# Performance work log

Measured on AMD Instinct MI355X. Metric: run time of the kernel, lower is better.

## Reference

```python
import jax, jax.numpy as jnp
import numpy as np

EPS = 1e-3  # BatchNorm eps from module init
N, C_IN, K = 200000, 256, 27
C_MID = C_IN // 4  # bottleneck expansion = 4


def batch_norm(h, gamma, beta):
    # BatchNorm1d in training mode: biased batch stats over the node dim
    mean = jnp.mean(h, axis=0)
    var = jnp.var(h, axis=0)
    return (h - mean) * jax.lax.rsqrt(var + EPS) * gamma + beta


def setup_inputs() -> dict:
    key = jax.random.key(0)
    ks = jax.random.split(key, 8)
    x = jax.random.normal(ks[0], (N, C_IN), dtype=jnp.float32)
    neigh = jax.random.randint(ks[1], (N, K), 0, N)  # 27-neighbor octree table
    # conv weights (no bias; BN follows). Fan-in scaled init.
    W1 = jax.random.normal(ks[2], (C_IN, C_MID), dtype=jnp.float32) / np.sqrt(C_IN)
    W2 = jax.random.normal(ks[3], (K, C_MID, C_MID), dtype=jnp.float32) / np.sqrt(K * C_MID)
    W3 = jax.random.normal(ks[4], (C_MID, C_IN), dtype=jnp.float32) / np.sqrt(C_MID)
    g1 = jnp.ones((C_MID,), jnp.float32); b1 = jnp.zeros((C_MID,), jnp.float32)
    g2 = jnp.ones((C_MID,), jnp.float32); b2 = jnp.zeros((C_MID,), jnp.float32)
    g3 = jnp.ones((C_IN,), jnp.float32); b3 = jnp.zeros((C_IN,), jnp.float32)
    return {"x": x, "neigh": neigh, "depth": 6,
            "W1": W1, "g1": g1, "b1": b1,
            "W2": W2, "g2": g2, "b2": b2,
            "W3": W3, "g3": g3, "b3": b3}


def reference(x, neigh, depth, W1, g1, b1, W2, g2, b2, W3, g3, b3):
    identity = x
    # conv_bn_relu1: 1x1 octree conv -> BN -> ReLU
    h = jax.nn.relu(batch_norm(x @ W1, g1, b1))  # [N, C_MID]
    # conv_bn_relu2: 3x3 octree conv (27-neighbor gather) -> BN -> ReLU
    gathered = h[neigh]                          # [N, 27, C_MID] irregular gather
    h = jnp.einsum('nkc,kcd->nd', gathered, W2)  # [N, C_MID]
    h = jax.nn.relu(batch_norm(h, g2, b2))
    # conv3: 1x1 octree conv back to C_IN, then BN + residual + ReLU
    h = batch_norm(h @ W3, g3, b3)               # [N, C_IN]
    return jax.nn.relu(h + identity)
```

## Files before the change

kernel.cpp:

```cpp
#include <hip/hip_runtime.h>
#include <stdint.h>

#define N_NODES 200000
#define C_INN   256
#define C_MIDD  64
#define KNB     27
#define MB_TILES 3125
#define GRAM_BLOCKS 512

typedef unsigned short u16;
typedef __attribute__((ext_vector_type(8))) short short8;
typedef __attribute__((ext_vector_type(4))) float floatx4;

__device__ inline float bf2f(u16 u) {
  union { uint32_t i; float f; } v; v.i = ((uint32_t)u) << 16; return v.f;
}
__device__ inline u16 f2bf(float f) {
  union { float f; uint32_t i; } v; v.f = f;
  uint32_t lsb = (v.i >> 16) & 1u;
  uint32_t r = v.i + 0x7fffu + lsb;
  return (u16)(r >> 16);
}

__global__ void prep_kernel(const float* __restrict__ W1, const float* __restrict__ W2,
                            const float* __restrict__ W3,
                            u16* __restrict__ w1t, u16* __restrict__ w2t,
                            u16* __restrict__ w3t, float* __restrict__ stats) {
  int tid = blockIdx.x * blockDim.x + threadIdx.x;
  int nth = gridDim.x * blockDim.x;
  for (int i = tid; i < 512; i += nth) stats[i] = 0.f;
  for (int i = tid; i < 256 * 64; i += nth) {
    int d = i >> 8, k = i & 255;
    w1t[i] = f2bf(W1[k * 64 + d]);
  }
  for (int i = tid; i < 27 * 64 * 64; i += nth) {
    int kn = i >> 12, r = i & 4095, d = r >> 6, c = r & 63;
    w2t[i] = f2bf(W2[kn * 4096 + c * 64 + d]);
  }
  for (int i = tid; i < 256 * 64; i += nth) {
    int d = i >> 6, k = i & 63;
    w3t[i] = f2bf(W3[k * 256 + d]);
  }
}

#define PAD1 136
__global__ __launch_bounds__(256) void gemm1_kernel(const float* __restrict__ x,
                                                    const u16* __restrict__ w1t,
                                                    u16* __restrict__ y1,
                                                    float* __restrict__ s) {
  __shared__ u16 Als[64 * PAD1];
  __shared__ u16 Bls[64 * PAD1];
  int t = threadIdx.x;
  long long rowBase = (long long)blockIdx.x * 64;
  int w = t >> 6, lane = t & 63;
  int m = lane & 15, q = lane >> 4;
  floatx4 acc[4] = {};

  for (int kh = 0; kh < 2; kh++) {
    if (kh) __syncthreads();
    #pragma unroll
    for (int j = 0; j < 8; j++) {
      int lin = j * 256 + t;
      int r = lin >> 5, c4 = lin & 31;
      floatx4 v = ((const floatx4*)x)[(rowBase + r) * 64 + kh * 32 + c4];
      ushort4 u;
      u.x = f2bf(v[0]); u.y = f2bf(v[1]); u.z = f2bf(v[2]); u.w = f2bf(v[3]);
      *(ushort4*)&Als[r * PAD1 + c4 * 4] = u;
    }
    #pragma unroll
    for (int j = 0; j < 4; j++) {
      int lin = j * 256 + t;
      int n = lin >> 4, c8 = lin & 15;
      uint4 u = ((const uint4*)w1t)[n * 32 + kh * 16 + c8];
      *(uint4*)&Bls[n * PAD1 + c8 * 8] = u;
    }
    __syncthreads();
    #pragma unroll
    for (int kc = 0; kc < 4; kc++) {
      short8 af = *(const short8*)&Als[(w * 16 + m) * PAD1 + kc * 32 + q * 8];
      #pragma unroll
      for (int tt = 0; tt < 4; tt++) {
        short8 bf = *(const short8*)&Bls[(tt * 16 + m) * PAD1 + kc * 32 + q * 8];
        acc[tt] = __builtin_amdgcn_mfma_f32_16x16x32_bf16(af, bf, acc[tt], 0, 0, 0);
      }
    }
  }
  long long base = rowBase + w * 16;
  #pragma unroll
  for (int tt = 0; tt < 4; tt++)
    #pragma unroll
    for (int r = 0; r < 4; r++)
      y1[(base + q * 4 + r) * 64 + tt * 16 + m] = f2bf(acc[tt][r]);

  float sv[4], qv[4];
  #pragma unroll
  for (int tt = 0; tt < 4; tt++) {
    float sl = 0.f, ql = 0.f;
    #pragma unroll
    for (int r = 0; r < 4; r++) { float v = acc[tt][r]; sl += v; ql += v * v; }
    sl += __shfl_xor(sl, 16); sl += __shfl_xor(sl, 32);
    ql += __shfl_xor(ql, 16); ql += __shfl_xor(ql, 32);
    sv[tt] = sl; qv[tt] = ql;
  }
  __syncthreads();
  float* sred = (float*)Als;
  float* qred = sred + 256;
  if (q == 0) {
    #pragma unroll
    for (int tt = 0; tt < 4; tt++) {
      sred[w * 64 + tt * 16 + m] = sv[tt];
      qred[w * 64 + tt * 16 + m] = qv[tt];
    }
  }
  __syncthreads();
  if (t < 64) {
    float S = 0.f, Q = 0.f;
    #pragma unroll
    for (int g = 0; g < 4; g++) { S += sred[g * 64 + t]; Q += qred[g * 64 + t]; }
    atomicAdd(&s[t], S);
    atomicAdd(&s[64 + t], Q);
  }
}

#define PAD2 72
__global__ __launch_bounds__(256) void gemm2_kernel(const u16* __restrict__ h1,
                                                    const int* __restrict__ neigh,
                                                    const u16* __restrict__ w2t,
                                                    u16* __restrict__ y2,
                                                    float* __restrict__ s) {
  __shared__ u16 Als[64 * PAD2];
  __shared__ u16 Bls[64 * PAD2];
  __shared__ int nidx[64 * 27];
  int t = threadIdx.x;
  long long rowBase = (long long)blockIdx.x * 64;
  #pragma unroll
  for (int j = 0; j < 7; j++) {
    int lin = j * 256 + t;
    if (lin < 64 * 27) nidx[lin] = neigh[rowBase * 27 + lin];
  }
  int w = t >> 6, lane = t & 63;
  int m = lane & 15, q = lane >> 4;
  floatx4 acc[4] = {};

  for (int k = 0; k < KNB; k++) {
    __syncthreads();
    #pragma unroll
    for (int j = 0; j < 2; j++) {
      int lin = j * 256 + t;
      int r = lin >> 3, c8 = lin & 7;
      long long src = (long long)nidx[r * 27 + k] * 8 + c8;
      *(uint4*)&Als[r * PAD2 + c8 * 8] = ((const uint4*)h1)[src];
      *(uint4*)&Bls[r * PAD2 + c8 * 8] = ((const uint4*)w2t)[k * 512 + lin];
    }
    __syncthreads();
    #pragma unroll
    for (int kc = 0; kc < 2; kc++) {
      short8 af = *(const short8*)&Als[(w * 16 + m) * PAD2 + kc * 32 + q * 8];
      #pragma unroll
      for (int tt = 0; tt < 4; tt++) {
        short8 bf = *(const short8*)&Bls[(tt * 16 + m) * PAD2 + kc * 32 + q * 8];
        acc[tt] = __builtin_amdgcn_mfma_f32_16x16x32_bf16(af, bf, acc[tt], 0, 0, 0);
      }
    }
  }
  long long base = rowBase + w * 16;
  #pragma unroll
  for (int tt = 0; tt < 4; tt++)
    #pragma unroll
    for (int r = 0; r < 4; r++)
      y2[(base + q * 4 + r) * 64 + tt * 16 + m] = f2bf(acc[tt][r]);

  float sv[4], qv[4];
  #pragma unroll
  for (int tt = 0; tt < 4; tt++) {
    float sl = 0.f, ql = 0.f;
    #pragma unroll
    for (int r = 0; r < 4; r++) { float v = acc[tt][r]; sl += v; ql += v * v; }
    sl += __shfl_xor(sl, 16); sl += __shfl_xor(sl, 32);
    ql += __shfl_xor(ql, 16); ql += __shfl_xor(ql, 32);
    sv[tt] = sl; qv[tt] = ql;
  }
  __syncthreads();
  float* sred = (float*)Als;
  float* qred = sred + 256;
  if (q == 0) {
    #pragma unroll
    for (int tt = 0; tt < 4; tt++) {
      sred[w * 64 + tt * 16 + m] = sv[tt];
      qred[w * 64 + tt * 16 + m] = qv[tt];
    }
  }
  __syncthreads();
  if (t < 64) {
    float S = 0.f, Q = 0.f;
    #pragma unroll
    for (int g = 0; g < 4; g++) { S += sred[g * 64 + t]; Q += qred[g * 64 + t]; }
    atomicAdd(&s[t], S);
    atomicAdd(&s[64 + t], Q);
  }
}

__global__ void finalize_kernel(const float* __restrict__ sums, const float* __restrict__ g,
                                const float* __restrict__ b, float* __restrict__ ac, int C) {
  int t = threadIdx.x;
  if (t < C) {
    float inv = 1.f / (float)N_NODES;
    float mean = sums[t] * inv;
    float var = sums[C + t] * inv - mean * mean;
    float a = g[t] * rsqrtf(var + 1e-3f);
    ac[t] = a;
    ac[C + t] = b[t] - mean * a;
  }
}

__global__ __launch_bounds__(256) void apply_bn_relu_kernel(u16* __restrict__ y,
                                                            const float* __restrict__ ac) {
  __shared__ float a[64], cc[64];
  int t = threadIdx.x;
  if (t < 64) { a[t] = ac[t]; cc[t] = ac[64 + t]; }
  __syncthreads();
  const long long total = (long long)N_NODES * 64 / 8;
  for (long long i = (long long)blockIdx.x * 256 + t; i < total;
       i += (long long)gridDim.x * 256) {
    uint4 u = ((uint4*)y)[i];
    int c0 = (int)((i & 7) * 8);
    u16* us = (u16*)&u;
    #pragma unroll
    for (int j = 0; j < 8; j++) {
      float v = bf2f(us[j]);
      v = fmaf(a[c0 + j], v, cc[c0 + j]);
      us[j] = f2bf(fmaxf(v, 0.f));
    }
    ((uint4*)y)[i] = u;
  }
}

#define PADG 72
__global__ __launch_bounds__(256) void gram_kernel(const u16* __restrict__ h2,
                                                   float* __restrict__ Gpart,
                                                   float* __restrict__ cspart) {
  __shared__ u16 T[64 * PADG];
  int t = threadIdx.x;
  int w = t >> 6, lane = t & 63;
  int m = lane & 15, q = lane >> 4;
  const int c8 = t & 7;
  floatx4 acc[4] = {};
  float csl[8] = {};
  for (int tile = blockIdx.x; tile < MB_TILES; tile += gridDim.x) {
    __syncthreads();
    #pragma unroll
    for (int j = 0; j < 2; j++) {
      int lin = j * 256 + t;
      int r = lin >> 3;
      uint4 u = ((const uint4*)h2)[(long long)tile * 512 + lin];
      u16* us = (u16*)&u;
      #pragma unroll
      for (int e = 0; e < 8; e++) {
        csl[e] += bf2f(us[e]);
        T[(c8 * 8 + e) * PADG + r] = us[e];
      }
    }
    __syncthreads();
    #pragma unroll
    for (int kc = 0; kc < 2; kc++) {
      short8 af = *(const short8*)&T[(w * 16 + m) * PADG + kc * 32 + q * 8];
      #pragma unroll
      for (int tt = 0; tt < 4; tt++) {
        short8 bf = *(const short8*)&T[(tt * 16 + m) * PADG + kc * 32 + q * 8];
        acc[tt] = __builtin_amdgcn_mfma_f32_16x16x32_bf16(af, bf, acc[tt], 0, 0, 0);
      }
    }
  }
  long long b = blockIdx.x;
  #pragma unroll
  for (int tt = 0; tt < 4; tt++)
    #pragma unroll
    for (int r = 0; r < 4; r++)
      Gpart[b * 4096 + (w * 16 + q * 4 + r) * 64 + tt * 16 + m] = acc[tt][r];
  __syncthreads();
  float* cred = (float*)T;
  #pragma unroll
  for (int e = 0; e < 8; e++) cred[t * 8 + e] = csl[e];
  __syncthreads();
  if (t < 64) {
    float S = 0.f;
    for (int g = 0; g < 32; g++) S += cred[((g << 3) | (t >> 3)) * 8 + (t & 7)];
    cspart[b * 64 + t] = S;
  }
}

__global__ void greduce_kernel(const float* __restrict__ Gpart,
                               const float* __restrict__ cspart,
                               float* __restrict__ G, float* __restrict__ cs) {
  int idx = blockIdx.x * 64 + threadIdx.x;
  if (idx < 4096) {
    float S = 0.f;
    for (int b = 0; b < GRAM_BLOCKS; b++) S += Gpart[b * 4096 + idx];
    G[idx] = S;
  } else if (idx < 4160) {
    int c = idx - 4096;
    float S = 0.f;
    for (int b = 0; b < GRAM_BLOCKS; b++) S += cspart[b * 64 + c];
    cs[c] = S;
  }
}

__global__ void finalize3_kernel(const float* __restrict__ G, const float* __restrict__ cs,
                                 const u16* __restrict__ w3t, const float* __restrict__ g3,
                                 const float* __restrict__ b3, float* __restrict__ ac3) {
  __shared__ float Gs[4096];
  __shared__ float css[64];
  int t = threadIdx.x;
  for (int i = t; i < 4096; i += 256) Gs[i] = G[i];
  if (t < 64) css[t] = cs[t];
  __syncthreads();
  float wv[64];
  #pragma unroll
  for (int k = 0; k < 64; k++) wv[k] = bf2f(w3t[t * 64 + k]);
  const float invN = 1.f / (float)N_NODES;
  float mean = 0.f;
  #pragma unroll
  for (int k = 0; k < 64; k++) mean += css[k] * wv[k];
  mean *= invN;
  float qf = 0.f;
  #pragma unroll
  for (int k = 0; k < 64; k++) {
    float tmp = 0.f;
    #pragma unroll
    for (int k2 = 0; k2 < 64; k2++) tmp += Gs[k * 64 + k2] * wv[k2];
    qf += wv[k] * tmp;
  }
  float var = qf * invN - mean * mean;
  float a = g3[t] * rsqrtf(var + 1e-3f);
  ac3[t] = a;
  ac3[256 + t] = b3[t] - mean * a;
}

#define PAD3 72
__global__ __launch_bounds__(256) void gemm3e_kernel(const u16* __restrict__ h2,
                                                     const u16* __restrict__ w3t,
                                                     const float* __restrict__ ac,
                                                     const float* __restrict__ x,
                                                     float* __restrict__ out) {
  __shared__ u16 Als[64 * PAD3];
  __shared__ u16 Bls[256 * PAD3];
  __shared__ __align__(16) float aS[256];
  __shared__ __align__(16) float cS[256];
  int t = threadIdx.x;
  aS[t] = ac[t]; cS[t] = ac[256 + t];
  long long rowBase = (long long)blockIdx.x * 64;
  #pragma unroll
  for (int j = 0; j < 2; j++) {
    int lin = j * 256 + t;
    int r = lin >> 3, c8 = lin & 7;
    *(uint4*)&Als[r * PAD3 + c8 * 8] = ((const uint4*)h2)[rowBase * 8 + lin];
  }
  #pragma unroll
  for (int j = 0; j < 8; j++) {
    int lin = j * 256 + t;
    int n = lin >> 3, c8 = lin & 7;
    *(uint4*)&Bls[n * PAD3 + c8 * 8] = ((const uint4*)w3t)[lin];
  }
  __syncthreads();
  int w = t >> 6, lane = t & 63;
  int m = lane & 15, q = lane >> 4;
  floatx4 acc[16] = {};
  short8 af0 = *(const short8*)&Als[(w * 16 + m) * PAD3 + q * 8];
  short8 af1 = *(const short8*)&Als[(w * 16 + m) * PAD3 + 32 + q * 8];
  #pragma unroll
  for (int tt = 0; tt < 16; tt++) {
    short8 b0 = *(const short8*)&Bls[(tt * 16 + m) * PAD3 + q * 8];
    short8 b1 = *(const short8*)&Bls[(tt * 16 + m) * PAD3 + 32 + q * 8];
    acc[tt] = __builtin_amdgcn_mfma_f32_16x16x32_bf16(b0, af0, acc[tt], 0, 0, 0);
    acc[tt] = __builtin_amdgcn_mfma_f32_16x16x32_bf16(b1, af1, acc[tt], 0, 0, 0);
  }
  long long row = rowBase + w * 16 + m;
  const floatx4* xr = (const floatx4*)x + row * 64;
  floatx4* outr = (floatx4*)out + row * 64;
  const floatx4* a4 = (const floatx4*)aS;
  const floatx4* c4 = (const floatx4*)cS;
  #pragma unroll
  for (int tt = 0; tt < 16; tt++) {
    int cq = tt * 4 + q;
    floatx4 xa = xr[cq];
    floatx4 av = a4[cq];
    floatx4 cv = c4[cq];
    floatx4 v;
    #pragma unroll
    for (int j = 0; j < 4; j++)
      v[j] = fmaxf(fmaf(av[j], acc[tt][j], cv[j]) + xa[j], 0.f);
    outr[cq] = v;
  }
}

extern "C" void kernel_launch(void* const* d_in, const int* in_sizes, int n_in,
                              void* d_out, int out_size, void* d_ws, size_t ws_size,
                              hipStream_t stream) {
  (void)in_sizes; (void)n_in; (void)out_size; (void)ws_size;
  const float* x  = (const float*)d_in[0];
  const int* neigh = (const int*)d_in[1];
  const float* W1 = (const float*)d_in[3];
  const float* g1 = (const float*)d_in[4];
  const float* b1 = (const float*)d_in[5];
  const float* W2 = (const float*)d_in[6];
  const float* g2 = (const float*)d_in[7];
  const float* b2 = (const float*)d_in[8];
  const float* W3 = (const float*)d_in[9];
  const float* g3 = (const float*)d_in[10];
  const float* b3 = (const float*)d_in[11];

  char* ws = (char*)d_ws;
  u16* h1  = (u16*)(ws);
  u16* h2  = (u16*)(ws + 25600000LL);
  u16* w1t = (u16*)(ws + 51200000LL);
  u16* w2t = (u16*)(ws + 51232768LL);
  u16* w3t = (u16*)(ws + 51453952LL);
  float* stats = (float*)(ws + 51486720LL);
  float* s1  = stats,       *ac1 = stats + 128;
  float* s2  = stats + 256, *ac2 = stats + 384;
  float* G   = stats + 512;
  float* cs3 = stats + 4608;
  float* ac3 = stats + 4672;
  float* Gpart  = (float*)(ws + 51507456LL);
  float* cspart = (float*)(ws + 59896064LL);
  float* out = (float*)d_out;

  prep_kernel<<<256, 256, 0, stream>>>(W1, W2, W3, w1t, w2t, w3t, stats);

  gemm1_kernel<<<MB_TILES, 256, 0, stream>>>(x, w1t, h1, s1);
  finalize_kernel<<<1, 256, 0, stream>>>(s1, g1, b1, ac1, 64);
  apply_bn_relu_kernel<<<2048, 256, 0, stream>>>(h1, ac1);

  gemm2_kernel<<<MB_TILES, 256, 0, stream>>>(h1, neigh, w2t, h2, s2);
  finalize_kernel<<<1, 256, 0, stream>>>(s2, g2, b2, ac2, 64);
  apply_bn_relu_kernel<<<2048, 256, 0, stream>>>(h2, ac2);

  gram_kernel<<<GRAM_BLOCKS, 256, 0, stream>>>(h2, Gpart, cspart);
  greduce_kernel<<<65, 64, 0, stream>>>(Gpart, cspart, G, cs3);
  finalize3_kernel<<<1, 256, 0, stream>>>(G, cs3, w3t, g3, b3, ac3);
  gemm3e_kernel<<<MB_TILES, 256, 0, stream>>>(h2, w3t, ac3, x, out);
}
```

Measured before the change: 691.5 us.

## Gather gemm2 operands directly into registers and fuse BN2+ReLU into consumers

The gemm2 kernel no longer stages gathered neighbor rows and W2 slices through shared memory with two barriers per neighbor. Each lane now loads its MFMA operand fragments straight from global memory, with W2 coming through cache. Separately, the standalone BN2+ReLU pass over h2 is removed, and the normalization plus ReLU is applied on the fly in the gram and gemm3 kernels. This saves one full read and write of h2 and the per-k synchronization, but it adds redundant uncoalesced global loads of W2 per wave and recomputes the BN affine twice.

```diff
diff --git a/kernel.cpp b/kernel.cpp
--- a/kernel.cpp
+++ b/kernel.cpp
@@ -122,15 +122,13 @@
   }
 }
 
-#define PAD2 72
 __global__ __launch_bounds__(256) void gemm2_kernel(const u16* __restrict__ h1,
                                                     const int* __restrict__ neigh,
                                                     const u16* __restrict__ w2t,
                                                     u16* __restrict__ y2,
                                                     float* __restrict__ s) {
-  __shared__ u16 Als[64 * PAD2];
-  __shared__ u16 Bls[64 * PAD2];
   __shared__ int nidx[64 * 27];
+  __shared__ float red[512];
   int t = threadIdx.x;
   long long rowBase = (long long)blockIdx.x * 64;
   #pragma unroll
@@ -140,27 +138,26 @@
   }
   int w = t >> 6, lane = t & 63;
   int m = lane & 15, q = lane >> 4;
+  int myrow = w * 16 + m;
+  __syncthreads();
   floatx4 acc[4] = {};
-
+  const u16* wbase = w2t + m * 64 + q * 8;
+  #pragma unroll 3
   for (int k = 0; k < KNB; k++) {
-    __syncthreads();
-    #pragma unroll
-    for (int j = 0; j < 2; j++) {
-      int lin = j * 256 + t;
-      int r = lin >> 3, c8 = lin & 7;
-      long long src = (long long)nidx[r * 27 + k] * 8 + c8;
-      *(uint4*)&Als[r * PAD2 + c8 * 8] = ((const uint4*)h1)[src];
-      *(uint4*)&Bls[r * PAD2 + c8 * 8] = ((const uint4*)w2t)[k * 512 + lin];
-    }
-    __syncthreads();
-    #pragma unroll
-    for (int kc = 0; kc < 2; kc++) {
-      short8 af = *(const short8*)&Als[(w * 16 + m) * PAD2 + kc * 32 + q * 8];
-      #pragma unroll
-      for (int tt = 0; tt < 4; tt++) {
-        short8 bf = *(const short8*)&Bls[(tt * 16 + m) * PAD2 + kc * 32 + q * 8];
-        acc[tt] = __builtin_amdgcn_mfma_f32_16x16x32_bf16(af, bf, acc[tt], 0, 0, 0);
-      }
+    long long src = (long long)nidx[myrow * 27 + k] * 64 + q * 8;
+    short8 a0 = *(const short8*)(h1 + src);
+    short8 a1 = *(const short8*)(h1 + src + 32);
+    const u16* wk = wbase + k * 4096;
+    short8 b0[4], b1[4];
+    #pragma unroll
+    for (int tt = 0; tt < 4; tt++) {
+      b0[tt] = *(const short8*)(wk + tt * 1024);
+      b1[tt] = *(const short8*)(wk + tt * 1024 + 32);
+    }
+    #pragma unroll
+    for (int tt = 0; tt < 4; tt++) {
+      acc[tt] = __builtin_amdgcn_mfma_f32_16x16x32_bf16(a0, b0[tt], acc[tt], 0, 0, 0);
+      acc[tt] = __builtin_amdgcn_mfma_f32_16x16x32_bf16(a1, b1[tt], acc[tt], 0, 0, 0);
     }
   }
   long long base = rowBase + w * 16;
@@ -180,9 +177,8 @@
     ql += __shfl_xor(ql, 16); ql += __shfl_xor(ql, 32);
     sv[tt] = sl; qv[tt] = ql;
   }
-  __syncthreads();
-  float* sred = (float*)Als;
-  float* qred = sred + 256;
+  float* sred = red;
+  float* qred = red + 256;
   if (q == 0) {
     #pragma unroll
     for (int tt = 0; tt < 4; tt++) {
@@ -237,6 +233,7 @@
 
 #define PADG 72
 __global__ __launch_bounds__(256) void gram_kernel(const u16* __restrict__ h2,
+                                                   const float* __restrict__ ac2,
                                                    float* __restrict__ Gpart,
                                                    float* __restrict__ cspart) {
   __shared__ u16 T[64 * PADG];
@@ -244,6 +241,12 @@
   int w = t >> 6, lane = t & 63;
   int m = lane & 15, q = lane >> 4;
   const int c8 = t & 7;
+  float a2r[8], c2r[8];
+  #pragma unroll
+  for (int e = 0; e < 8; e++) {
+    a2r[e] = ac2[c8 * 8 + e];
+    c2r[e] = ac2[64 + c8 * 8 + e];
+  }
   floatx4 acc[4] = {};
   float csl[8] = {};
   for (int tile = blockIdx.x; tile < MB_TILES; tile += gridDim.x) {
@@ -256,8 +259,10 @@
       u16* us = (u16*)&u;
       #pragma unroll
       for (int e = 0; e < 8; e++) {
-        csl[e] += bf2f(us[e]);
-        T[(c8 * 8 + e) * PADG + r] = us[e];
+        float v = fmaxf(fmaf(a2r[e], bf2f(us[e]), c2r[e]), 0.f);
+        u16 nb = f2bf(v);
+        csl[e] += bf2f(nb);
+        T[(c8 * 8 + e) * PADG + r] = nb;
       }
     }
     __syncthreads();
@@ -339,6 +344,7 @@
 #define PAD3 72
 __global__ __launch_bounds__(256) void gemm3e_kernel(const u16* __restrict__ h2,
                                                      const u16* __restrict__ w3t,
+                                                     const float* __restrict__ ac2,
                                                      const float* __restrict__ ac,
                                                      const float* __restrict__ x,
                                                      float* __restrict__ out) {
@@ -349,11 +355,23 @@
   int t = threadIdx.x;
   aS[t] = ac[t]; cS[t] = ac[256 + t];
   long long rowBase = (long long)blockIdx.x * 64;
+  const int c8t = t & 7;
+  float a2r[8], c2r[8];
+  #pragma unroll
+  for (int e = 0; e < 8; e++) {
+    a2r[e] = ac2[c8t * 8 + e];
+    c2r[e] = ac2[64 + c8t * 8 + e];
+  }
   #pragma unroll
   for (int j = 0; j < 2; j++) {
     int lin = j * 256 + t;
-    int r = lin >> 3, c8 = lin & 7;
-    *(uint4*)&Als[r * PAD3 + c8 * 8] = ((const uint4*)h2)[rowBase * 8 + lin];
+    int r = lin >> 3;
+    uint4 u = ((const uint4*)h2)[rowBase * 8 + lin];
+    u16* us = (u16*)&u;
+    #pragma unroll
+    for (int e = 0; e < 8; e++)
+      us[e] = f2bf(fmaxf(fmaf(a2r[e], bf2f(us[e]), c2r[e]), 0.f));
+    *(uint4*)&Als[r * PAD3 + c8t * 8] = u;
   }
   #pragma unroll
   for (int j = 0; j < 8; j++) {
@@ -433,10 +451,9 @@
 
   gemm2_kernel<<<MB_TILES, 256, 0, stream>>>(h1, neigh, w2t, h2, s2);
   finalize_kernel<<<1, 256, 0, stream>>>(s2, g2, b2, ac2, 64);
-  apply_bn_relu_kernel<<<2048, 256, 0, stream>>>(h2, ac2);
-
-  gram_kernel<<<GRAM_BLOCKS, 256, 0, stream>>>(h2, Gpart, cspart);
+
+  gram_kernel<<<GRAM_BLOCKS, 256, 0, stream>>>(h2, ac2, Gpart, cspart);
   greduce_kernel<<<65, 64, 0, stream>>>(Gpart, cspart, G, cs3);
   finalize3_kernel<<<1, 256, 0, stream>>>(G, cs3, w3t, g3, b3, ac3);
-  gemm3e_kernel<<<MB_TILES, 256, 0, stream>>>(h2, w3t, ac3, x, out);
-}
+  gemm3e_kernel<<<MB_TILES, 256, 0, stream>>>(h2, w3t, ac2, ac3, x, out);
+}
```

Measured after the change: 950.8 us. 37.5% more time.
